# Performance work log

Measured on AMD Instinct MI355X. Metric: run time of the kernel, lower is better.

Reference implementation:

```python
import math
import jax, jax.numpy as jnp
import numpy as np

V = 50257
R_MAX = 3.0
LAMBDA_RADIAL = 0.1
T = 1.0
LOG_V = math.log(V)
EPS = 1e-12


def _project_to_hyperboloid(sp):
    # sp: [..., n] spatial part; x0 = sqrt(1 + ||sp||^2) satisfies Lorentz constraint
    x0 = jnp.sqrt(1.0 + jnp.sum(sp * sp, axis=-1, keepdims=True))
    return jnp.concatenate([x0, sp], axis=-1)


def setup_inputs() -> dict:
    key = jax.random.key(0)
    k1, k2, k3, k4 = jax.random.split(key, 4)
    B, L, n = 2, 1024, 768
    h_student = _project_to_hyperboloid(0.5 * jax.random.normal(k1, (B, L, n), dtype=jnp.float32))
    W_vocab = _project_to_hyperboloid(0.5 * jax.random.normal(k2, (V, n), dtype=jnp.float32))
    p_raw = jax.random.uniform(k3, (B, L, V), dtype=jnp.float32) + 1e-6
    p_teacher = p_raw / jnp.sum(p_raw, axis=-1, keepdims=True)
    teacher_entropy = jax.random.uniform(k4, (B, L), dtype=jnp.float32) * LOG_V
    return {"h_student": h_student, "W_vocab": W_vocab, "p_teacher": p_teacher, "teacher_entropy": teacher_entropy}


def _decompose(h):
    # Lorentz log-map at origin: v = [0, arccosh(x0) * sp/||sp||]
    # -> r = arccosh(x0), u = sp / ||sp||
    x0 = jnp.clip(h[..., 0], 1.0 + 1e-7, None)
    sp = h[..., 1:]
    r = jnp.arccosh(x0)
    u = sp / jnp.clip(jnp.linalg.norm(sp, axis=-1, keepdims=True), EPS)
    return r, u


def reference(h_student, W_vocab, p_teacher, teacher_entropy):
    r_s, u_s = _decompose(h_student)          # [B,L], [B,L,n]
    _, u_w = _decompose(W_vocab)              # [V,n]
    cos_logits = jnp.einsum('bln,vn->blv', u_s, u_w)  # [B,L,V] via GEMM
    log_p_ang = jax.nn.log_softmax(cos_logits / T, axis=-1)
    B, L, Vv = cos_logits.shape
    # F.kl_div(log_q, p, 'batchmean') = sum(p*(log p - log q)) / (B*L)
    kl = jnp.sum(p_teacher * (jnp.log(jnp.clip(p_teacher, EPS)) - log_p_ang)) / (B * L)
    l_angular = kl * (T ** 2)
    H_norm = jnp.clip(teacher_entropy / LOG_V, 0.0, 1.0)
    r_target = jax.nn.sigmoid(-H_norm) * R_MAX
    l_radial = jnp.mean((r_s - jax.lax.stop_gradient(r_target)) ** 2)
    l_total = l_angular + LAMBDA_RADIAL * l_radial
    return jnp.stack([l_total, l_angular, l_radial, jnp.mean(r_s), jnp.mean(r_target), jnp.mean(H_norm)])
```

## Files before the change

### kernel.cpp

```cpp
#include <hip/hip_runtime.h>
#include <hip/hip_bf16.h>

#define V_SIZE 50257
#define V_PAD  50304
#define NDIM   768
#define NROWS  2048
#define BM 128
#define BN 128
#define BK 32
#define KSTEPS (NDIM / BK)
#define LOG_V_F 10.824905119f
#define EPS_F   1e-12f

typedef __bf16 bf16x8 __attribute__((ext_vector_type(8)));
typedef float  f32x4  __attribute__((ext_vector_type(4)));

__device__ __forceinline__ void async16(const void* g, void* l) {
  __builtin_amdgcn_global_load_lds(
      (const __attribute__((address_space(1))) void*)g,
      (__attribute__((address_space(3))) void*)l, 16, 0, 0);
}

__global__ __launch_bounds__(256)
void normalize_rows_k(const float* __restrict__ src,
                      __hip_bfloat16* __restrict__ dst,
                      float* __restrict__ r_out,
                      int nrows_src)
{
  const int row = blockIdx.x;
  const int t = threadIdx.x;
  __shared__ float red[8];
  if (row >= nrows_src) {
    __hip_bfloat16 z = __float2bfloat16(0.0f);
    dst[(size_t)row * NDIM + t]       = z;
    dst[(size_t)row * NDIM + t + 256] = z;
    dst[(size_t)row * NDIM + t + 512] = z;
    return;
  }
  const float* h = src + (size_t)row * (NDIM + 1);
  float v0 = h[1 + t], v1 = h[1 + t + 256], v2 = h[1 + t + 512];
  float ss = v0 * v0 + v1 * v1 + v2 * v2;
  #pragma unroll
  for (int m = 1; m < 64; m <<= 1) ss += __shfl_xor(ss, m, 64);
  const int w = t >> 6;
  if ((t & 63) == 0) red[w] = ss;
  __syncthreads();
  if (t == 0) {
    float tot = red[0] + red[1] + red[2] + red[3];
    red[4] = 1.0f / fmaxf(sqrtf(tot), 1e-12f);
    if (r_out) {
      float x0 = fmaxf(h[0], 1.0f + 1e-7f);
      r_out[row] = acoshf(x0);
    }
  }
  __syncthreads();
  const float inv = red[4];
  dst[(size_t)row * NDIM + t]       = __float2bfloat16(v0 * inv);
  dst[(size_t)row * NDIM + t + 256] = __float2bfloat16(v1 * inv);
  dst[(size_t)row * NDIM + t + 512] = __float2bfloat16(v2 * inv);
}

__global__ __launch_bounds__(256, 2)
void fused_gemm_kl(const __hip_bfloat16* __restrict__ uS,
                   const __hip_bfloat16* __restrict__ uW,
                   const float* __restrict__ p_teacher,
                   float* __restrict__ sum_exp,
                   float* __restrict__ S_scalar)
{
  __shared__ __attribute__((aligned(16))) __hip_bfloat16 lA[BM * BK];
  __shared__ __attribute__((aligned(16))) __hip_bfloat16 lB[BN * BK];
  __shared__ float sred[4];

  const int t = threadIdx.x;
  const int lane = t & 63;
  const int w = t >> 6;
  const int wr = w >> 1, wc = w & 1;
  const int rowBase = blockIdx.x * BM;
  const int colBase = blockIdx.y * BN;

  f32x4 acc[4][4];
  #pragma unroll
  for (int i = 0; i < 4; ++i)
    #pragma unroll
    for (int j = 0; j < 4; ++j) acc[i][j] = (f32x4){0.f, 0.f, 0.f, 0.f};

  const char* gA = (const char*)uS;
  const char* gB = (const char*)uW;
  const int b0 = w * 1024 + lane * 16;
  const int r0 = b0 >> 6, kb0 = b0 & 63;
  const int b1 = 4096 + b0;
  const int r1 = b1 >> 6, kb1 = b1 & 63;
  const char* srcA0 = gA + (size_t)(rowBase + r0) * (NDIM * 2) + kb0;
  const char* srcA1 = gA + (size_t)(rowBase + r1) * (NDIM * 2) + kb1;
  const char* srcB0 = gB + (size_t)(colBase + r0) * (NDIM * 2) + kb0;
  const char* srcB1 = gB + (size_t)(colBase + r1) * (NDIM * 2) + kb1;
  char* ldsA0 = (char*)lA + w * 1024;
  char* ldsA1 = (char*)lA + 4096 + w * 1024;
  char* ldsB0 = (char*)lB + w * 1024;
  char* ldsB1 = (char*)lB + 4096 + w * 1024;

  for (int kk = 0; kk < KSTEPS; ++kk) {
    if (kk) __syncthreads();
    const size_t ko = (size_t)kk * (BK * 2);
    async16(srcA0 + ko, ldsA0);
    async16(srcA1 + ko, ldsA1);
    async16(srcB0 + ko, ldsB0);
    async16(srcB1 + ko, ldsB1);
    __syncthreads();

    bf16x8 af[4], bfr[4];
    #pragma unroll
    for (int mi = 0; mi < 4; ++mi) {
      int arow = wr * 64 + mi * 16 + (lane & 15);
      af[mi] = *(const bf16x8*)((const char*)lA + arow * 64 + (lane >> 4) * 16);
    }
    #pragma unroll
    for (int ni = 0; ni < 4; ++ni) {
      int brow = wc * 64 + ni * 16 + (lane & 15);
      bfr[ni] = *(const bf16x8*)((const char*)lB + brow * 64 + (lane >> 4) * 16);
    }
    #pragma unroll
    for (int mi = 0; mi < 4; ++mi)
      #pragma unroll
      for (int ni = 0; ni < 4; ++ni)
        acc[mi][ni] = __builtin_amdgcn_mfma_f32_16x16x32_bf16(
            af[mi], bfr[ni], acc[mi][ni], 0, 0, 0);
  }

  float sacc = 0.0f;
  const int cgrp = lane >> 4;
  const int cidx = lane & 15;
  #pragma unroll
  for (int mi = 0; mi < 4; ++mi) {
    float esum[4] = {0.f, 0.f, 0.f, 0.f};
    const int row0 = rowBase + wr * 64 + mi * 16 + cgrp * 4;
    #pragma unroll
    for (int ni = 0; ni < 4; ++ni) {
      const int v = colBase + wc * 64 + ni * 16 + cidx;
      const bool valid = (v < V_SIZE);
      const float* prow = p_teacher + (size_t)row0 * V_SIZE + v;
      #pragma unroll
      for (int j = 0; j < 4; ++j) {
        float logit = acc[mi][ni][j];
        if (valid) {
          float p = prow[(size_t)j * V_SIZE];
          float lp = __logf(fmaxf(p, EPS_F));
          sacc = fmaf(p, lp - logit, sacc);
          esum[j] += __expf(logit);
        }
      }
    }
    #pragma unroll
    for (int j = 0; j < 4; ++j) {
      float e = esum[j];
      e += __shfl_xor(e, 1, 64);
      e += __shfl_xor(e, 2, 64);
      e += __shfl_xor(e, 4, 64);
      e += __shfl_xor(e, 8, 64);
      if (cidx == 0) atomicAdd(&sum_exp[row0 + j], e);
    }
  }
  #pragma unroll
  for (int m = 1; m < 64; m <<= 1) sacc += __shfl_xor(sacc, m, 64);
  if (lane == 0) sred[w] = sacc;
  __syncthreads();
  if (t == 0) atomicAdd(S_scalar, sred[0] + sred[1] + sred[2] + sred[3]);
}

__global__ __launch_bounds__(256)
void finalize_k(const float* __restrict__ sum_exp,
                const float* __restrict__ S_scalar,
                const float* __restrict__ r_s,
                const float* __restrict__ te,
                float* __restrict__ out)
{
  const int t = threadIdx.x;
  float lse = 0.f, sq = 0.f, rs = 0.f, rt = 0.f, hn = 0.f;
  for (int row = t; row < NROWS; row += 256) {
    lse += __logf(sum_exp[row]);
    float r = r_s[row];
    float h = fminf(fmaxf(te[row] / LOG_V_F, 0.0f), 1.0f);
    float rtar = 3.0f / (1.0f + expf(h));
    sq += (r - rtar) * (r - rtar);
    rs += r; rt += rtar; hn += h;
  }
  #pragma unroll
  for (int m = 1; m < 64; m <<= 1) {
    lse += __shfl_xor(lse, m, 64);
    sq  += __shfl_xor(sq, m, 64);
    rs  += __shfl_xor(rs, m, 64);
    rt  += __shfl_xor(rt, m, 64);
    hn  += __shfl_xor(hn, m, 64);
  }
  __shared__ float red[5][4];
  const int w = t >> 6;
  if ((t & 63) == 0) { red[0][w]=lse; red[1][w]=sq; red[2][w]=rs; red[3][w]=rt; red[4][w]=hn; }
  __syncthreads();
  if (t == 0) {
    float L  = red[0][0]+red[0][1]+red[0][2]+red[0][3];
    float SQ = red[1][0]+red[1][1]+red[1][2]+red[1][3];
    float RS = red[2][0]+red[2][1]+red[2][2]+red[2][3];
    float RT = red[3][0]+red[3][1]+red[3][2]+red[3][3];
    float HN = red[4][0]+red[4][1]+red[4][2]+red[4][3];
    float kl = (S_scalar[0] + L) / (float)NROWS;
    float l_rad = SQ / (float)NROWS;
    out[0] = kl + 0.1f * l_rad;
    out[1] = kl;
    out[2] = l_rad;
    out[3] = RS / (float)NROWS;
    out[4] = RT / (float)NROWS;
    out[5] = HN / (float)NROWS;
  }
}

extern "C" void kernel_launch(void* const* d_in, const int* in_sizes, int n_in,
                              void* d_out, int out_size, void* d_ws, size_t ws_size,
                              hipStream_t stream) {
  const float* h_student = (const float*)d_in[0];
  const float* W_vocab   = (const float*)d_in[1];
  const float* p_teacher = (const float*)d_in[2];
  const float* te        = (const float*)d_in[3];
  float* out = (float*)d_out;

  char* ws = (char*)d_ws;
  __hip_bfloat16* uW = (__hip_bfloat16*)ws;
  size_t off = (size_t)V_PAD * NDIM * 2;
  __hip_bfloat16* uS = (__hip_bfloat16*)(ws + off); off += (size_t)NROWS * NDIM * 2;
  float* r_s     = (float*)(ws + off); off += NROWS * 4;
  float* sum_exp = (float*)(ws + off); off += NROWS * 4;
  float* S_scalar = (float*)(ws + off);

  hipMemsetAsync(sum_exp, 0, NROWS * 4 + 16, stream);

  normalize_rows_k<<<dim3(V_PAD), dim3(256), 0, stream>>>(W_vocab, uW, nullptr, V_SIZE);
  normalize_rows_k<<<dim3(NROWS), dim3(256), 0, stream>>>(h_student, uS, r_s, NROWS);
  fused_gemm_kl<<<dim3(NROWS / BM, V_PAD / BN), dim3(256), 0, stream>>>(
      uS, uW, p_teacher, sum_exp, S_scalar);
  finalize_k<<<1, 256, 0, stream>>>(sum_exp, S_scalar, r_s, te, out);
}
```

Baseline: 948.4 us.

## Prefetch teacher probabilities during last GEMM step; one-wave-per-row normalize

The fused GEMM+KL kernel now issues the global loads of p_teacher for the first output sub-tile together with the last k-step's LDS loads. It uses a manual vmcnt wait and barrier so the final MFMA step overlaps those loads, then double-buffers the p_teacher loads for the following sub-tiles. Invalid columns are handled by a multiplicative mask with clamped indices instead of a branch, which removes divergence. The normalize kernel assigns one wave per row with shuffle-only reduction, dropping shared memory and block barriers. The cost is higher register use (two 16-float buffers) under the 2-block launch bound, and a hand-written waitcnt that depends on the compiler's instruction order.

New measurement: 834.0 us. -12.1%, faster.

```diff
diff --git a/kernel.cpp b/kernel.cpp
--- a/kernel.cpp
+++ b/kernel.cpp
@@ -22,42 +22,36 @@
 }
 
 __global__ __launch_bounds__(256)
-void normalize_rows_k(const float* __restrict__ src,
-                      __hip_bfloat16* __restrict__ dst,
-                      float* __restrict__ r_out,
-                      int nrows_src)
+void normalize_rows_wave(const float* __restrict__ src,
+                         __hip_bfloat16* __restrict__ dst,
+                         float* __restrict__ r_out,
+                         int nrows_src, int nrows_dst)
 {
-  const int row = blockIdx.x;
-  const int t = threadIdx.x;
-  __shared__ float red[8];
-  if (row >= nrows_src) {
-    __hip_bfloat16 z = __float2bfloat16(0.0f);
-    dst[(size_t)row * NDIM + t]       = z;
-    dst[(size_t)row * NDIM + t + 256] = z;
-    dst[(size_t)row * NDIM + t + 512] = z;
+  const int wid = blockIdx.x * 4 + (threadIdx.x >> 6);
+  const int lane = threadIdx.x & 63;
+  if (wid >= nrows_dst) return;
+  __hip_bfloat16* drow = dst + (size_t)wid * NDIM;
+  if (wid >= nrows_src) {
+    #pragma unroll
+    for (int s = 0; s < 12; ++s) drow[s * 64 + lane] = __float2bfloat16(0.0f);
     return;
   }
-  const float* h = src + (size_t)row * (NDIM + 1);
-  float v0 = h[1 + t], v1 = h[1 + t + 256], v2 = h[1 + t + 512];
-  float ss = v0 * v0 + v1 * v1 + v2 * v2;
+  const float* h = src + (size_t)wid * (NDIM + 1);
+  float v[12];
+  float ss = 0.0f;
+  #pragma unroll
+  for (int s = 0; s < 12; ++s) {
+    v[s] = h[1 + s * 64 + lane];
+    ss = fmaf(v[s], v[s], ss);
+  }
   #pragma unroll
   for (int m = 1; m < 64; m <<= 1) ss += __shfl_xor(ss, m, 64);
-  const int w = t >> 6;
-  if ((t & 63) == 0) red[w] = ss;
-  __syncthreads();
-  if (t == 0) {
-    float tot = red[0] + red[1] + red[2] + red[3];
-    red[4] = 1.0f / fmaxf(sqrtf(tot), 1e-12f);
-    if (r_out) {
-      float x0 = fmaxf(h[0], 1.0f + 1e-7f);
-      r_out[row] = acoshf(x0);
-    }
-  }
-  __syncthreads();
-  const float inv = red[4];
-  dst[(size_t)row * NDIM + t]       = __float2bfloat16(v0 * inv);
-  dst[(size_t)row * NDIM + t + 256] = __float2bfloat16(v1 * inv);
-  dst[(size_t)row * NDIM + t + 512] = __float2bfloat16(v2 * inv);
+  const float inv = 1.0f / fmaxf(sqrtf(ss), 1e-12f);
+  if (r_out != nullptr && lane == 0)
+    r_out[wid] = acoshf(fmaxf(h[0], 1.0f + 1e-7f));
+  #pragma unroll
+  for (int s = 0; s < 12; ++s)
+    drow[s * 64 + lane] = __float2bfloat16(v[s] * inv);
 }
 
 __global__ __launch_bounds__(256, 2)
@@ -99,15 +93,14 @@
   char* ldsB0 = (char*)lB + w * 1024;
   char* ldsB1 = (char*)lB + 4096 + w * 1024;
 
-  for (int kk = 0; kk < KSTEPS; ++kk) {
-    if (kk) __syncthreads();
+  auto stage = [&](int kk) {
     const size_t ko = (size_t)kk * (BK * 2);
     async16(srcA0 + ko, ldsA0);
     async16(srcA1 + ko, ldsA1);
     async16(srcB0 + ko, ldsB0);
     async16(srcB1 + ko, ldsB1);
-    __syncthreads();
-
+  };
+  auto compute = [&]() {
     bf16x8 af[4], bfr[4];
     #pragma unroll
     for (int mi = 0; mi < 4; ++mi) {
@@ -125,29 +118,64 @@
       for (int ni = 0; ni < 4; ++ni)
         acc[mi][ni] = __builtin_amdgcn_mfma_f32_16x16x32_bf16(
             af[mi], bfr[ni], acc[mi][ni], 0, 0, 0);
-  }
-
-  float sacc = 0.0f;
+  };
+
+  for (int kk = 0; kk < KSTEPS - 1; ++kk) {
+    if (kk) __syncthreads();
+    stage(kk);
+    __syncthreads();
+    compute();
+  }
+
   const int cgrp = lane >> 4;
   const int cidx = lane & 15;
+  float vmaskf[4];
+  int   vcol[4];
+  #pragma unroll
+  for (int ni = 0; ni < 4; ++ni) {
+    int v = colBase + wc * 64 + ni * 16 + cidx;
+    vmaskf[ni] = (v < V_SIZE) ? 1.0f : 0.0f;
+    vcol[ni]   = (v < V_SIZE) ? v : (V_SIZE - 1);
+  }
+  auto pload = [&](int mi, float* pr) {
+    const int row0 = rowBase + wr * 64 + mi * 16 + cgrp * 4;
+    #pragma unroll
+    for (int ni = 0; ni < 4; ++ni) {
+      const float* pp = p_teacher + (size_t)row0 * V_SIZE + vcol[ni];
+      #pragma unroll
+      for (int j = 0; j < 4; ++j) pr[ni * 4 + j] = pp[(size_t)j * V_SIZE];
+    }
+  };
+
+  float prA[16], prB[16];
+
+  __syncthreads();
+  stage(KSTEPS - 1);
+  __builtin_amdgcn_sched_barrier(0);
+  pload(0, prA);
+  __builtin_amdgcn_sched_barrier(0);
+  asm volatile("s_waitcnt vmcnt(16)" ::: "memory");
+  __builtin_amdgcn_s_barrier();
+  __builtin_amdgcn_sched_barrier(0);
+  compute();
+
+  float sacc = 0.0f;
   #pragma unroll
   for (int mi = 0; mi < 4; ++mi) {
+    float* cur = (mi & 1) ? prB : prA;
+    float* nxt = (mi & 1) ? prA : prB;
+    if (mi < 3) pload(mi + 1, nxt);
+    const int row0 = rowBase + wr * 64 + mi * 16 + cgrp * 4;
     float esum[4] = {0.f, 0.f, 0.f, 0.f};
-    const int row0 = rowBase + wr * 64 + mi * 16 + cgrp * 4;
     #pragma unroll
     for (int ni = 0; ni < 4; ++ni) {
-      const int v = colBase + wc * 64 + ni * 16 + cidx;
-      const bool valid = (v < V_SIZE);
-      const float* prow = p_teacher + (size_t)row0 * V_SIZE + v;
+      const float m = vmaskf[ni];
       #pragma unroll
       for (int j = 0; j < 4; ++j) {
         float logit = acc[mi][ni][j];
-        if (valid) {
-          float p = prow[(size_t)j * V_SIZE];
-          float lp = __logf(fmaxf(p, EPS_F));
-          sacc = fmaf(p, lp - logit, sacc);
-          esum[j] += __expf(logit);
-        }
+        float p = cur[ni * 4 + j] * m;
+        sacc = fmaf(p, __logf(fmaxf(p, EPS_F)) - logit, sacc);
+        esum[j] = fmaf(m, __expf(logit), esum[j]);
       }
     }
     #pragma unroll
@@ -232,8 +260,10 @@
 
   hipMemsetAsync(sum_exp, 0, NROWS * 4 + 16, stream);
 
-  normalize_rows_k<<<dim3(V_PAD), dim3(256), 0, stream>>>(W_vocab, uW, nullptr, V_SIZE);
-  normalize_rows_k<<<dim3(NROWS), dim3(256), 0, stream>>>(h_student, uS, r_s, NROWS);
+  normalize_rows_wave<<<dim3(V_PAD / 4), dim3(256), 0, stream>>>(
+      W_vocab, uW, nullptr, V_SIZE, V_PAD);
+  normalize_rows_wave<<<dim3(NROWS / 4), dim3(256), 0, stream>>>(
+      h_student, uS, r_s, NROWS, NROWS);
   fused_gemm_kl<<<dim3(NROWS / BM, V_PAD / BN), dim3(256), 0, stream>>>(
       uS, uW, p_teacher, sum_exp, S_scalar);
   finalize_k<<<1, 256, 0, stream>>>(sum_exp, S_scalar, r_s, te, out);
```
